# Kernel optimization log

Hardware: AMD Instinct MI355X
Metric: run time of the kernel (lower is better)

The kernel has to match this reference:

```python
import jax, jax.numpy as jnp
import numpy as np

LEAKY_SLOPE = 0.2
MASK_VAL = -9e15


def setup_inputs() -> dict:
    key = jax.random.key(0)
    k1, k2, k3, k4, k5, k6 = jax.random.split(key, 6)
    N_ex, N_kc, F_in, F_out = 20000, 1024, 128, 128
    exercise_h = jax.random.normal(k1, (N_ex, F_in), dtype=jnp.float32)
    kc_h = jax.random.normal(k2, (N_kc, F_in), dtype=jnp.float32)
    adj_exercise_kc = jax.random.randint(k3, (N_ex, N_kc), 0, 2, dtype=jnp.int32)
    # learned params (kaiming-ish scale)
    W1 = jax.random.normal(k4, (F_in, F_out), dtype=jnp.float32) * np.sqrt(2.0 / F_in)
    E = jax.random.normal(k5, (F_in, F_out), dtype=jnp.float32) * np.sqrt(2.0 / F_in)
    a = jax.random.normal(k6, (2 * F_out, 1), dtype=jnp.float32) * np.sqrt(2.0 / (2 * F_out))
    return {"exercise_h": exercise_h, "kc_h": kc_h,
            "adj_exercise_kc": adj_exercise_kc, "W1": W1, "E": E, "a": a}


def reference(exercise_h, kc_h, adj_exercise_kc, W1, E, a):
    F_out = W1.shape[1]
    kc_Wh = kc_h @ W1              # [N_kc, F_out]
    ex_Wh = exercise_h @ W1        # [N_ex, F_out]
    # Decompose a into halves: cat([ex_Wh_i, kc_Wh_j]) @ a == ex_Wh_i@a1 + kc_Wh_j@a2.
    a1, a2 = a[:F_out, 0], a[F_out:, 0]
    e = jax.nn.leaky_relu(ex_Wh @ a1[:, None] + (kc_Wh @ a2)[None, :],
                          negative_slope=LEAKY_SLOPE)   # [N_ex, N_kc]
    e = jnp.where(adj_exercise_kc > 0, e, MASK_VAL)
    attention = jax.nn.softmax(e, axis=1)
    new_kc_embed = attention @ kc_Wh               # [N_ex, F_out]
    exercise_Eh = exercise_h @ E                   # mode == 2
    return jax.nn.elu(new_kc_embed * exercise_Eh)
```

## Files before the change

kernel.cpp:

```cpp
#include <hip/hip_runtime.h>
#include <math.h>

#define N_EXC   20000
#define N_KCC   1024
#define FDIM    128
#define LEAKY_S 0.2f

#define BR  32
#define TJ  128
#define EXS 136

typedef unsigned short ushort_t;
typedef __attribute__((ext_vector_type(8))) short short8;
typedef __attribute__((ext_vector_type(4))) float floatx4;

__device__ __forceinline__ ushort_t f2bf(float f) {
    unsigned u = __float_as_uint(f);
    u += 0x7FFF + ((u >> 16) & 1);
    return (ushort_t)(u >> 16);
}

__device__ __forceinline__ void async16(const void* g, void* l) {
    __builtin_amdgcn_global_load_lds(
        (const __attribute__((address_space(1))) unsigned int*)g,
        (__attribute__((address_space(3))) unsigned int*)l,
        16, 0, 0);
}


__global__ __launch_bounds__(256) void gat_prep(const float* __restrict__ kc_h,
                                                const float* __restrict__ W1,
                                                const float* __restrict__ E,
                                                const float* __restrict__ a,
                                                float* __restrict__ ws)
{
    float* tarr = ws;
    float* w1a1 = ws + N_KCC;
    ushort_t* kc_sw = (ushort_t*)(ws + N_KCC + FDIM);
    ushort_t* E_sw  = kc_sw + FDIM * N_KCC;
    const int tid = threadIdx.x;
    const int b = blockIdx.x;

    __shared__ __align__(16) float kct[128 * 132];
    __shared__ __align__(16) ushort_t sw[32 * 128];
    __shared__ __align__(16) float w1a2_lds[FDIM];

    if (b < 32) {
        const int jb = b >> 2, fq = b & 3;
        const float* kcbase = kc_h + (size_t)jb * 128 * FDIM;
        #pragma unroll
        for (int u = 0; u < 16; ++u) {
            int flat = u * 256 + tid;
            int r = flat >> 5, c4 = (flat & 31) * 4;
            float4 v = *(const float4*)(kcbase + r * FDIM + c4);
            kct[r * 132 + c4 + 0] = v.x; kct[r * 132 + c4 + 1] = v.y;
            kct[r * 132 + c4 + 2] = v.z; kct[r * 132 + c4 + 3] = v.w;
        }
        __syncthreads();
        const int jg = tid >> 4;
        const int fg = tid & 15;
        const int f0 = fq * 32 + fg * 2;
        float acc[8][2];
        #pragma unroll
        for (int i = 0; i < 8; ++i) { acc[i][0] = 0.f; acc[i][1] = 0.f; }
        for (int k4 = 0; k4 < FDIM; k4 += 4) {
            float4 av[8];
            #pragma unroll
            for (int i = 0; i < 8; ++i)
                av[i] = *(const float4*)(kct + (jg * 8 + i) * 132 + k4);
            #pragma unroll
            for (int kk = 0; kk < 4; ++kk) {
                float2 bv = *(const float2*)(W1 + (k4 + kk) * FDIM + f0);
                #pragma unroll
                for (int i = 0; i < 8; ++i) {
                    float a_ = ((const float*)&av[i])[kk];
                    acc[i][0] += a_ * bv.x;
                    acc[i][1] += a_ * bv.y;
                }
            }
        }
        #pragma unroll
        for (int c = 0; c < 2; ++c) {
            int f = f0 + c;
            int fl = fg * 2 + c;
            unsigned pk[4];
            #pragma unroll
            for (int i = 0; i < 4; ++i)
                pk[i] = (unsigned)f2bf(acc[2 * i][c]) | ((unsigned)f2bf(acc[2 * i + 1][c]) << 16);
            int cp = jg ^ (f & 15);
            *(uint4*)(sw + fl * 128 + cp * 8) = make_uint4(pk[0], pk[1], pk[2], pk[3]);
        }
        __syncthreads();
        ushort_t* dst = kc_sw + ((size_t)jb * 128 + fq * 32) * 128;
        #pragma unroll
        for (int u = 0; u < 2; ++u) {
            int flat = u * 256 + tid;
            *(uint4*)(dst + flat * 8) = *(const uint4*)(sw + flat * 8);
        }
        return;
    }

    if (b < 36) {
        if (tid >= 128) {
            int k = tid - 128;
            float acc = 0.f;
            const float* row = W1 + k * FDIM;
            #pragma unroll 8
            for (int f = 0; f < FDIM; ++f) acc += row[f] * a[FDIM + f];
            w1a2_lds[k] = acc;
        } else if (b == 32) {
            float acc = 0.f;
            const float* row = W1 + tid * FDIM;
            #pragma unroll 8
            for (int f = 0; f < FDIM; ++f) acc += row[f] * a[f];
            w1a1[tid] = acc;
        }
        __syncthreads();
        int j = (b - 32) * 256 + tid;
        float s = 0.f;
        #pragma unroll 8
        for (int c = 0; c < 32; ++c) {
            float4 v = *(const float4*)(kc_h + (size_t)j * FDIM + c * 4);
            s += v.x * w1a2_lds[c * 4 + 0] + v.y * w1a2_lds[c * 4 + 1]
               + v.z * w1a2_lds[c * 4 + 2] + v.w * w1a2_lds[c * 4 + 3];
        }
        tarr[j] = s;
        return;
    }

    #pragma unroll
    for (int u = 0; u < 8; ++u) {
        int ch = u * 256 + tid;
        int n = ch >> 4, cp = ch & 15;
        int c = cp ^ (n & 15);
        unsigned pk[4];
        #pragma unroll
        for (int i = 0; i < 4; ++i) {
            float e0 = E[(c * 8 + 2 * i + 0) * FDIM + n];
            float e1 = E[(c * 8 + 2 * i + 1) * FDIM + n];
            pk[i] = (unsigned)f2bf(e0) | ((unsigned)f2bf(e1) << 16);
        }
        *(uint4*)(E_sw + ch * 8) = make_uint4(pk[0], pk[1], pk[2], pk[3]);
    }
}

__global__ __launch_bounds__(256, 3) void gat_main(const float* __restrict__ ex_h,
                                                   const int* __restrict__ adj,
                                                   const float* __restrict__ ws,
                                                   float* __restrict__ out)
{
    const float* tarr = ws;
    const float* w1a1 = ws + N_KCC;
    const ushort_t* kc_sw = (const ushort_t*)(ws + N_KCC + FDIM);
    const ushort_t* E_sw  = kc_sw + FDIM * N_KCC;

    __shared__ __align__(16) float t_lds[N_KCC];
    __shared__ __align__(16) ushort_t kc_lds[FDIM * TJ];
    __shared__ __align__(16) ushort_t exw_lds[BR * EXS];
    __shared__ __align__(16) float scrA[256];
    __shared__ __align__(16) float scrB[256];
    __shared__ float w1a1_lds[FDIM];
    __shared__ float s_lds[BR], m_lds[BR], denom_lds[BR];

    const int tid  = threadIdx.x;
    const int R0   = blockIdx.x * BR;
    const int lane = tid & 63, wid = tid >> 6;
    const int l15  = lane & 15, quad = lane >> 4;

    #pragma unroll
    for (int u = 0; u < 8; ++u) {
        int ci = u * 256 + tid;
        async16(E_sw + ci * 8, kc_lds + ci * 8);
    }

    #pragma unroll
    for (int u = 0; u < 4; ++u) t_lds[u * 256 + tid] = tarr[u * 256 + tid];
    if (tid < FDIM) w1a1_lds[tid] = w1a1[tid];
    const int r0 = tid >> 3;
    const int fc = (tid & 7) * 16;
    float exv[16];
    {
        const float* src = ex_h + (size_t)(R0 + r0) * FDIM + fc;
        #pragma unroll
        for (int c = 0; c < 4; ++c) {
            float4 v = *(const float4*)(src + c * 4);
            exv[c * 4 + 0] = v.x; exv[c * 4 + 1] = v.y;
            exv[c * 4 + 2] = v.z; exv[c * 4 + 3] = v.w;
        }
        unsigned pk[8];
        #pragma unroll
        for (int i = 0; i < 8; ++i)
            pk[i] = (unsigned)f2bf(exv[2 * i]) | ((unsigned)f2bf(exv[2 * i + 1]) << 16);
        *(uint4*)(exw_lds + r0 * EXS + fc)     = make_uint4(pk[0], pk[1], pk[2], pk[3]);
        *(uint4*)(exw_lds + r0 * EXS + fc + 8) = make_uint4(pk[4], pk[5], pk[6], pk[7]);
    }
    __syncthreads();

    {
        float mx = fmaxf(fmaxf(t_lds[tid], t_lds[256 + tid]),
                         fmaxf(t_lds[512 + tid], t_lds[768 + tid]));
        scrB[tid] = mx;
        float p = 0.f;
        #pragma unroll
        for (int i = 0; i < 16; ++i) p += exv[i] * w1a1_lds[fc + i];
        scrA[tid] = p;
    }
    __syncthreads();
    if (tid < 64)
        scrB[tid] = fmaxf(fmaxf(scrB[tid], scrB[tid + 64]),
                          fmaxf(scrB[tid + 128], scrB[tid + 192]));
    __syncthreads();
    if (tid < BR) {
        float Tm = scrB[0];
        #pragma unroll 8
        for (int i = 1; i < 64; ++i) Tm = fmaxf(Tm, scrB[i]);
        float s = 0.f;
        #pragma unroll
        for (int g = 0; g < 8; ++g) s += scrA[tid * 8 + g];
        s_lds[tid] = s;
        float x = s + Tm;
        m_lds[tid] = (x >= 0.f) ? x : LEAKY_S * x;
    }
    __syncthreads();

    floatx4 eh_acc[2][2], att_acc[2][2];
    #pragma unroll
    for (int mg = 0; mg < 2; ++mg)
        #pragma unroll
        for (int h = 0; h < 2; ++h) {
            eh_acc[mg][h]  = (floatx4){0.f, 0.f, 0.f, 0.f};
            att_acc[mg][h] = (floatx4){0.f, 0.f, 0.f, 0.f};
        }
    #pragma unroll
    for (int kk = 0; kk < 4; ++kk) {
        short8 a0 = *(const short8*)(exw_lds + l15 * EXS + kk * 32 + quad * 8);
        short8 a1 = *(const short8*)(exw_lds + (16 + l15) * EXS + kk * 32 + quad * 8);
        #pragma unroll
        for (int h = 0; h < 2; ++h) {
            const int n = (h * 4 + wid) * 16 + l15;
            const int cp = (kk * 4 + quad) ^ l15;
            short8 bf = *(const short8*)(kc_lds + n * TJ + cp * 8);
            eh_acc[0][h] = __builtin_amdgcn_mfma_f32_16x16x32_bf16(a0, bf, eh_acc[0][h], 0, 0, 0);
            eh_acc[1][h] = __builtin_amdgcn_mfma_f32_16x16x32_bf16(a1, bf, eh_acc[1][h], 0, 0, 0);
        }
    }

    const int r_w = tid >> 3;
    const int jg  = tid & 7;
    const float sr = s_lds[r_w];
    const float mr = m_lds[r_w];
    float denom_part = 0.f;
    const int* aptr = adj + (size_t)(R0 + r_w) * N_KCC + jg * 16;
    int4 cur0 = *(const int4*)(aptr + 0);
    int4 cur1 = *(const int4*)(aptr + 4);
    int4 cur2 = *(const int4*)(aptr + 8);
    int4 cur3 = *(const int4*)(aptr + 12);

    for (int jt = 0; jt < N_KCC / TJ; ++jt) {
        const int j0 = jt * TJ;
        __syncthreads();
        {
            const ushort_t* gsrc = kc_sw + (size_t)jt * (FDIM * TJ);
            #pragma unroll
            for (int u = 0; u < 8; ++u) {
                int ci = u * 256 + tid;
                async16(gsrc + ci * 8, kc_lds + ci * 8);
            }
        }
        {
            const int jb = j0 + jg * 16;
            int av[16] = {cur0.x, cur0.y, cur0.z, cur0.w, cur1.x, cur1.y, cur1.z, cur1.w,
                          cur2.x, cur2.y, cur2.z, cur2.w, cur3.x, cur3.y, cur3.z, cur3.w};
            float wv[16];
            #pragma unroll
            for (int c = 0; c < 4; ++c) {
                float4 t4 = *(const float4*)(t_lds + jb + c * 4);
                float tv[4] = {t4.x, t4.y, t4.z, t4.w};
                #pragma unroll
                for (int e = 0; e < 4; ++e) {
                    float x = sr + tv[e];
                    x = fmaxf(x, LEAKY_S * x);
                    float w = __expf(x - mr);
                    w = (av[c * 4 + e] > 0) ? w : 0.f;
                    denom_part += w;
                    wv[c * 4 + e] = w;
                }
            }
            unsigned pk[8];
            #pragma unroll
            for (int i = 0; i < 8; ++i) {
                unsigned ua = __float_as_uint(wv[2 * i + 0]) + 0x8000u;
                unsigned ub = __float_as_uint(wv[2 * i + 1]) + 0x8000u;
                pk[i] = __builtin_amdgcn_perm(ub, ua, 0x07060302);
            }
            *(uint4*)(exw_lds + r_w * EXS + jg * 16)     = make_uint4(pk[0], pk[1], pk[2], pk[3]);
            *(uint4*)(exw_lds + r_w * EXS + jg * 16 + 8) = make_uint4(pk[4], pk[5], pk[6], pk[7]);
        }
        __syncthreads();
        {
            int jn = (jt + 1 < N_KCC / TJ) ? (jt + 1) * TJ : jt * TJ;
            cur0 = *(const int4*)(aptr + jn + 0);
            cur1 = *(const int4*)(aptr + jn + 4);
            cur2 = *(const int4*)(aptr + jn + 8);
            cur3 = *(const int4*)(aptr + jn + 12);
        }
        #pragma unroll
        for (int kk = 0; kk < 4; ++kk) {
            short8 a0 = *(const short8*)(exw_lds + l15 * EXS + kk * 32 + quad * 8);
            short8 a1 = *(const short8*)(exw_lds + (16 + l15) * EXS + kk * 32 + quad * 8);
            #pragma unroll
            for (int h = 0; h < 2; ++h) {
                const int f = (h * 4 + wid) * 16 + l15;
                const int cp = (kk * 4 + quad) ^ l15;
                short8 bf = *(const short8*)(kc_lds + f * TJ + cp * 8);
                att_acc[0][h] = __builtin_amdgcn_mfma_f32_16x16x32_bf16(a0, bf, att_acc[0][h], 0, 0, 0);
                att_acc[1][h] = __builtin_amdgcn_mfma_f32_16x16x32_bf16(a1, bf, att_acc[1][h], 0, 0, 0);
            }
        }
    }

    __syncthreads();
    scrA[tid] = denom_part;
    __syncthreads();
    if (tid < BR) {
        float d = 0.f;
        #pragma unroll
        for (int g = 0; g < 8; ++g) d += scrA[tid * 8 + g];
        denom_lds[tid] = (d > 0.f) ? d : 1.f;
    }
    __syncthreads();

    #pragma unroll
    for (int mg = 0; mg < 2; ++mg) {
        float rd[4];
        #pragma unroll
        for (int reg = 0; reg < 4; ++reg)
            rd[reg] = 1.f / denom_lds[mg * 16 + quad * 4 + reg];
        #pragma unroll
        for (int h = 0; h < 2; ++h) {
            const int col = (h * 4 + wid) * 16 + l15;
            #pragma unroll
            for (int reg = 0; reg < 4; ++reg) {
                const int rl = mg * 16 + quad * 4 + reg;
                float v = att_acc[mg][h][reg] * rd[reg] * eh_acc[mg][h][reg];
                out[(size_t)(R0 + rl) * FDIM + col] = (v > 0.f) ? v : expm1f(v);
            }
        }
    }
}

extern "C" void kernel_launch(void* const* d_in, const int* in_sizes, int n_in,
                              void* d_out, int out_size, void* d_ws, size_t ws_size,
                              hipStream_t stream)
{
    const float* ex_h = (const float*)d_in[0];
    const float* kc_h = (const float*)d_in[1];
    const int*   adj  = (const int*)d_in[2];
    const float* W1   = (const float*)d_in[3];
    const float* E    = (const float*)d_in[4];
    const float* a    = (const float*)d_in[5];
    float* outp = (float*)d_out;
    float* ws   = (float*)d_ws;

    gat_prep<<<37, 256, 0, stream>>>(kc_h, W1, E, a, ws);
    gat_main<<<N_EXC / BR, 256, 0, stream>>>(ex_h, adj, ws, outp);
}
```

Before: 157.2 us.

## Precompute global key max in prep, fold log2e, and overlap adjacency prefetch

The prep kernel now scales the attention logit terms by log2(e) and writes per-block maxima of the key term, so the main kernel no longer reduces the 1024-entry max and can use exp2 with a precomputed fused max/fma argument. The main loop swaps __syncthreads for raw barriers with a partial vmcnt wait, so the next adjacency tile's loads stay in flight across the MFMA phase. It also raises wave priority during the MFMAs and moves the first adjacency loads earlier. The hand-placed waitcnt depends on the compiler's load ordering, and if that ordering shifts the async LDS fill may not be complete at the barrier.

New measurement: 156.7 us. Within noise of the previous version (-0.3%).

```diff
diff --git a/kernel.cpp b/kernel.cpp
--- a/kernel.cpp
+++ b/kernel.cpp
@@ -5,6 +5,7 @@
 #define N_KCC   1024
 #define FDIM    128
 #define LEAKY_S 0.2f
+#define LOG2E   1.44269504f
 
 #define BR  32
 #define TJ  128
@@ -27,6 +28,8 @@
         16, 0, 0);
 }
 
+#define WS_TMAX (N_KCC + FDIM)
+#define WS_KC   (N_KCC + FDIM + 8)
 
 __global__ __launch_bounds__(256) void gat_prep(const float* __restrict__ kc_h,
                                                 const float* __restrict__ W1,
@@ -34,9 +37,10 @@
                                                 const float* __restrict__ a,
                                                 float* __restrict__ ws)
 {
-    float* tarr = ws;
-    float* w1a1 = ws + N_KCC;
-    ushort_t* kc_sw = (ushort_t*)(ws + N_KCC + FDIM);
+    float* tarr  = ws;
+    float* w1a1  = ws + N_KCC;
+    float* tmax4 = ws + WS_TMAX;
+    ushort_t* kc_sw = (ushort_t*)(ws + WS_KC);
     ushort_t* E_sw  = kc_sw + FDIM * N_KCC;
     const int tid = threadIdx.x;
     const int b = blockIdx.x;
@@ -44,6 +48,7 @@
     __shared__ __align__(16) float kct[128 * 132];
     __shared__ __align__(16) ushort_t sw[32 * 128];
     __shared__ __align__(16) float w1a2_lds[FDIM];
+    __shared__ float redm[4];
 
     if (b < 32) {
         const int jb = b >> 2, fq = b & 3;
@@ -113,7 +118,7 @@
             const float* row = W1 + tid * FDIM;
             #pragma unroll 8
             for (int f = 0; f < FDIM; ++f) acc += row[f] * a[f];
-            w1a1[tid] = acc;
+            w1a1[tid] = acc * LOG2E;
         }
         __syncthreads();
         int j = (b - 32) * 256 + tid;
@@ -124,7 +129,15 @@
             s += v.x * w1a2_lds[c * 4 + 0] + v.y * w1a2_lds[c * 4 + 1]
                + v.z * w1a2_lds[c * 4 + 2] + v.w * w1a2_lds[c * 4 + 3];
         }
-        tarr[j] = s;
+        float t2 = s * LOG2E;
+        tarr[j] = t2;
+        float bm = t2;
+        #pragma unroll
+        for (int off = 32; off; off >>= 1) bm = fmaxf(bm, __shfl_xor(bm, off));
+        if ((tid & 63) == 0) redm[tid >> 6] = bm;
+        __syncthreads();
+        if (tid == 0)
+            tmax4[b - 32] = fmaxf(fmaxf(redm[0], redm[1]), fmaxf(redm[2], redm[3]));
         return;
     }
 
@@ -149,18 +162,18 @@
                                                    const float* __restrict__ ws,
                                                    float* __restrict__ out)
 {
-    const float* tarr = ws;
-    const float* w1a1 = ws + N_KCC;
-    const ushort_t* kc_sw = (const ushort_t*)(ws + N_KCC + FDIM);
+    const float* tarr  = ws;
+    const float* w1a1  = ws + N_KCC;
+    const float* tmax4 = ws + WS_TMAX;
+    const ushort_t* kc_sw = (const ushort_t*)(ws + WS_KC);
     const ushort_t* E_sw  = kc_sw + FDIM * N_KCC;
 
     __shared__ __align__(16) float t_lds[N_KCC];
     __shared__ __align__(16) ushort_t kc_lds[FDIM * TJ];
     __shared__ __align__(16) ushort_t exw_lds[BR * EXS];
     __shared__ __align__(16) float scrA[256];
-    __shared__ __align__(16) float scrB[256];
     __shared__ float w1a1_lds[FDIM];
-    __shared__ float s_lds[BR], m_lds[BR], denom_lds[BR];
+    __shared__ float a_lds[BR], b_lds[BR], denom_lds[BR];
 
     const int tid  = threadIdx.x;
     const int R0   = blockIdx.x * BR;
@@ -197,31 +210,35 @@
     __syncthreads();
 
     {
-        float mx = fmaxf(fmaxf(t_lds[tid], t_lds[256 + tid]),
-                         fmaxf(t_lds[512 + tid], t_lds[768 + tid]));
-        scrB[tid] = mx;
         float p = 0.f;
         #pragma unroll
         for (int i = 0; i < 16; ++i) p += exv[i] * w1a1_lds[fc + i];
         scrA[tid] = p;
     }
     __syncthreads();
-    if (tid < 64)
-        scrB[tid] = fmaxf(fmaxf(scrB[tid], scrB[tid + 64]),
-                          fmaxf(scrB[tid + 128], scrB[tid + 192]));
-    __syncthreads();
     if (tid < BR) {
-        float Tm = scrB[0];
-        #pragma unroll 8
-        for (int i = 1; i < 64; ++i) Tm = fmaxf(Tm, scrB[i]);
-        float s = 0.f;
-        #pragma unroll
-        for (int g = 0; g < 8; ++g) s += scrA[tid * 8 + g];
-        s_lds[tid] = s;
-        float x = s + Tm;
-        m_lds[tid] = (x >= 0.f) ? x : LEAKY_S * x;
-    }
-    __syncthreads();
+        float s2 = 0.f;
+        #pragma unroll
+        for (int g = 0; g < 8; ++g) s2 += scrA[tid * 8 + g];
+        float Tm2 = fmaxf(fmaxf(tmax4[0], tmax4[1]), fmaxf(tmax4[2], tmax4[3]));
+        float x2 = s2 + Tm2;
+        float m2 = fmaxf(x2, LEAKY_S * x2);
+        a_lds[tid] = s2 - m2;
+        b_lds[tid] = fmaf(s2, LEAKY_S, -m2);
+    }
+    __syncthreads();
+
+    const int r_w = tid >> 3;
+    const int jg  = tid & 7;
+    const float ar = a_lds[r_w];
+    const float br = b_lds[r_w];
+    float denom_part = 0.f;
+    const int* aptr = adj + (size_t)(R0 + r_w) * N_KCC + jg * 16;
+
+    int4 cur0 = *(const int4*)(aptr + 0);
+    int4 cur1 = *(const int4*)(aptr + 4);
+    int4 cur2 = *(const int4*)(aptr + 8);
+    int4 cur3 = *(const int4*)(aptr + 12);
 
     floatx4 eh_acc[2][2], att_acc[2][2];
     #pragma unroll
@@ -245,20 +262,10 @@
         }
     }
 
-    const int r_w = tid >> 3;
-    const int jg  = tid & 7;
-    const float sr = s_lds[r_w];
-    const float mr = m_lds[r_w];
-    float denom_part = 0.f;
-    const int* aptr = adj + (size_t)(R0 + r_w) * N_KCC + jg * 16;
-    int4 cur0 = *(const int4*)(aptr + 0);
-    int4 cur1 = *(const int4*)(aptr + 4);
-    int4 cur2 = *(const int4*)(aptr + 8);
-    int4 cur3 = *(const int4*)(aptr + 12);
-
     for (int jt = 0; jt < N_KCC / TJ; ++jt) {
         const int j0 = jt * TJ;
-        __syncthreads();
+        asm volatile("" ::: "memory");
+        __builtin_amdgcn_s_barrier();
         {
             const ushort_t* gsrc = kc_sw + (size_t)jt * (FDIM * TJ);
             #pragma unroll
@@ -267,6 +274,7 @@
                 async16(gsrc + ci * 8, kc_lds + ci * 8);
             }
         }
+        asm volatile("" ::: "memory");
         {
             const int jb = j0 + jg * 16;
             int av[16] = {cur0.x, cur0.y, cur0.z, cur0.w, cur1.x, cur1.y, cur1.z, cur1.w,
@@ -278,14 +286,21 @@
                 float tv[4] = {t4.x, t4.y, t4.z, t4.w};
                 #pragma unroll
                 for (int e = 0; e < 4; ++e) {
-                    float x = sr + tv[e];
-                    x = fmaxf(x, LEAKY_S * x);
-                    float w = __expf(x - mr);
+                    float t2 = tv[e];
+                    float arg = fmaxf(ar + t2, fmaf(t2, LEAKY_S, br));
+                    float w = exp2f(arg);
                     w = (av[c * 4 + e] > 0) ? w : 0.f;
                     denom_part += w;
                     wv[c * 4 + e] = w;
                 }
             }
+            {
+                int jn = ((jt + 1) & 7) * TJ;
+                cur0 = *(const int4*)(aptr + jn + 0);
+                cur1 = *(const int4*)(aptr + jn + 4);
+                cur2 = *(const int4*)(aptr + jn + 8);
+                cur3 = *(const int4*)(aptr + jn + 12);
+            }
             unsigned pk[8];
             #pragma unroll
             for (int i = 0; i < 8; ++i) {
@@ -296,14 +311,9 @@
             *(uint4*)(exw_lds + r_w * EXS + jg * 16)     = make_uint4(pk[0], pk[1], pk[2], pk[3]);
             *(uint4*)(exw_lds + r_w * EXS + jg * 16 + 8) = make_uint4(pk[4], pk[5], pk[6], pk[7]);
         }
-        __syncthreads();
-        {
-            int jn = (jt + 1 < N_KCC / TJ) ? (jt + 1) * TJ : jt * TJ;
-            cur0 = *(const int4*)(aptr + jn + 0);
-            cur1 = *(const int4*)(aptr + jn + 4);
-            cur2 = *(const int4*)(aptr + jn + 8);
-            cur3 = *(const int4*)(aptr + jn + 12);
-        }
+        asm volatile("s_waitcnt vmcnt(4) lgkmcnt(0)" ::: "memory");
+        __builtin_amdgcn_s_barrier();
+        __builtin_amdgcn_s_setprio(1);
         #pragma unroll
         for (int kk = 0; kk < 4; ++kk) {
             short8 a0 = *(const short8*)(exw_lds + l15 * EXS + kk * 32 + quad * 8);
@@ -317,6 +327,7 @@
                 att_acc[1][h] = __builtin_amdgcn_mfma_f32_16x16x32_bf16(a1, bf, att_acc[1][h], 0, 0, 0);
             }
         }
+        __builtin_amdgcn_s_setprio(0);
     }
 
     __syncthreads();
```
